# Kernel tuning notes

Measured on AMD Instinct MI355X. Metric: run time of the kernel, lower is better.

Reference implementation:

```python
import jax, jax.numpy as jnp
import numpy as np

EMBED_DIM = 2048
HEAD_DIM = 128
B, T = 4, 2048


def setup_inputs() -> dict:
    key = jax.random.key(0)
    k1, k2, k3, k4 = jax.random.split(key, 4)
    x_in = jax.random.normal(k1, (B, T, EMBED_DIM), dtype=jnp.float32)
    scale = 1.0 / np.sqrt(EMBED_DIM)
    Wq = jax.random.normal(k2, (EMBED_DIM, HEAD_DIM), dtype=jnp.float32) * scale
    Wk = jax.random.normal(k3, (EMBED_DIM, HEAD_DIM), dtype=jnp.float32) * scale
    Wv = jax.random.normal(k4, (EMBED_DIM, HEAD_DIM), dtype=jnp.float32) * scale
    return {"x_in": x_in, "Wq": Wq, "Wk": Wk, "Wv": Wv}


def reference(x_in, Wq, Wk, Wv):
    # x_in: [B, T, E]; projections (Linear, no bias)
    q = jnp.einsum('bte,ed->btd', x_in, Wq)  # [B,T,D]
    k = jnp.einsum('bte,ed->btd', x_in, Wk)
    v = jnp.einsum('bte,ed->btd', x_in, Wv)
    t = x_in.shape[1]
    d = Wq.shape[1]
    s = jnp.einsum('btd,bsd->bts', q, k) / jnp.sqrt(jnp.asarray(d, q.dtype))  # [B,Tq,Tk]
    # causal mask: positions with tril==0 (k index > q index) -> -inf
    causal = jnp.tril(jnp.ones((t, t), dtype=bool))
    s = jnp.where(causal, s, -jnp.inf)
    # NOTE: original module applies softmax over dim=1 (query axis), faithfully reproduced
    a = jax.nn.softmax(s, axis=1)
    z = jnp.einsum('bts,bsd->btd', a, v)  # [B,T,D]
    return z
```

## Files before the change

### kernel.cpp

```cpp
#include <hip/hip_runtime.h>

typedef _Float16 f16x8 __attribute__((ext_vector_type(8)));
typedef float f32x4 __attribute__((ext_vector_type(4)));

#define T_DIM 2048
#define E_DIM 2048
#define D_DIM 128
#define NB 4
#define KSP_P 4
#define KCH_P 512
#define KSP_A 8
#define KCH_A 256
#define CH2 64
#define NCH2 (T_DIM / CH2)

__device__ __forceinline__ void gll16(const void* g, void* l) {
  __builtin_amdgcn_global_load_lds(
      (const __attribute__((address_space(1))) unsigned int*)g,
      (__attribute__((address_space(3))) unsigned int*)l, 16, 0, 0);
}

__device__ __forceinline__ void merge_stat(float& m, float& l, float pm, float pl) {
  if (pm != -__builtin_inff()) {
    float nm = fmaxf(m, pm);
    l = l * __expf(m - nm) + pl * __expf(pm - nm);
    m = nm;
  }
}


__global__ void cvt_w(const float* __restrict__ Wq, const float* __restrict__ Wk,
                      const float* __restrict__ Wv, _Float16* __restrict__ WhT) {
  int idx = blockIdx.x * 256 + threadIdx.x;
  int w = blockIdx.y;
  const float* W = (w == 0) ? Wq : ((w == 1) ? Wk : Wv);
  int e = idx & (E_DIM - 1), d = idx >> 11;
  WhT[(size_t)w * (D_DIM * E_DIM) + idx] = (_Float16)W[e * D_DIM + d];
}


__global__ __launch_bounds__(256) void proj_gemm(
    const float* __restrict__ x, const _Float16* __restrict__ WhT,
    _Float16* __restrict__ Ph) {
  __shared__ _Float16 As[128 * 32];
  __shared__ _Float16 Bs[128 * 32];
  const int tid = threadIdx.x, w = tid >> 6, lane = tid & 63;
  const int wr = w >> 1, wc = w & 1, quad = lane >> 4, l16 = lane & 15;
  const int t0 = blockIdx.x * 128;
  const int wsel = blockIdx.y, ks = blockIdx.z;
  const _Float16* B = WhT + (size_t)wsel * (D_DIM * E_DIM);
  const int srow = lane >> 2, scol = (lane & 3) * 8;
  f32x4 acc[4][4] = {};
  for (int k0 = ks * KCH_P; k0 < ks * KCH_P + KCH_P; k0 += 32) {
    __syncthreads();
#pragma unroll
    for (int q = 0; q < 2; ++q) {
      int rbase = w * 32 + q * 16;
      int row = rbase + srow;
      const float* xp = x + (size_t)(t0 + row) * E_DIM + k0 + scol;
      f32x4 a0 = *(const f32x4*)xp;
      f32x4 a1 = *(const f32x4*)(xp + 4);
      f16x8 o;
#pragma unroll
      for (int e = 0; e < 4; ++e) { o[e] = (_Float16)a0[e]; o[e + 4] = (_Float16)a1[e]; }
      *(f16x8*)(As + row * 32 + scol) = o;
      gll16(B + (size_t)row * E_DIM + k0 + scol, Bs + rbase * 32);
    }
    __syncthreads();
    f16x8 af[4], bf[4];
#pragma unroll
    for (int i = 0; i < 4; ++i)
      af[i] = *(const f16x8*)(As + (wr * 64 + i * 16 + l16) * 32 + quad * 8);
#pragma unroll
    for (int j = 0; j < 4; ++j)
      bf[j] = *(const f16x8*)(Bs + (wc * 64 + j * 16 + l16) * 32 + quad * 8);
#pragma unroll
    for (int i = 0; i < 4; ++i)
#pragma unroll
      for (int j = 0; j < 4; ++j)
        acc[i][j] = __builtin_amdgcn_mfma_f32_16x16x32_f16(af[i], bf[j], acc[i][j], 0, 0, 0);
  }
  _Float16* P = Ph + ((size_t)(ks * 3 + wsel) << 20);
#pragma unroll
  for (int i = 0; i < 4; ++i)
#pragma unroll
    for (int j = 0; j < 4; ++j) {
      int n = wc * 64 + j * 16 + l16;
#pragma unroll
      for (int r = 0; r < 4; ++r) {
        int t = t0 + wr * 64 + i * 16 + quad * 4 + r;
        _Float16 h = (_Float16)acc[i][j][r];
        if (wsel < 2) P[(size_t)t * D_DIM + n] = h;
        else P[((size_t)(t >> 11) * D_DIM + n) * T_DIM + (t & (T_DIM - 1))] = h;
      }
    }
}


__global__ void proj_reduce(const _Float16* __restrict__ Ph, _Float16* __restrict__ Qh,
                            _Float16* __restrict__ Kh, _Float16* __restrict__ VT) {
  size_t u = ((size_t)blockIdx.x * 256 + threadIdx.x) * 8;
  int mat = (int)(u >> 20);
  size_t rem = u & ((1u << 20) - 1);
  float s[8] = {};
#pragma unroll
  for (int ks = 0; ks < KSP_P; ++ks) {
    f16x8 p = *(const f16x8*)(Ph + ((size_t)(ks * 3 + mat) << 20) + rem);
#pragma unroll
    for (int e = 0; e < 8; ++e) s[e] += (float)p[e];
  }
  f16x8 o;
#pragma unroll
  for (int e = 0; e < 8; ++e) o[e] = (_Float16)s[e];
  _Float16* dst = (mat == 0) ? Qh : ((mat == 1) ? Kh : VT);
  *(f16x8*)(dst + rem) = o;
}


__global__ __launch_bounds__(256) void s_gemm(const _Float16* __restrict__ Qh,
                                              const _Float16* __restrict__ Kh,
                                              _Float16* __restrict__ S,
                                              float* __restrict__ Pm,
                                              float* __restrict__ Pl) {
  int idx = blockIdx.x;
  int xt = (int)((sqrtf(8.f * idx + 1.f) - 1.f) * 0.5f);
  while ((xt + 1) * (xt + 2) / 2 <= idx) ++xt;
  while (xt * (xt + 1) / 2 > idx) --xt;
  int yt = idx - xt * (xt + 1) / 2;
  __shared__ _Float16 As[128 * 32];
  __shared__ _Float16 Bs[128 * 32];
  const int tid = threadIdx.x, w = tid >> 6, lane = tid & 63;
  const int wr = w >> 1, wc = w & 1, quad = lane >> 4, l16 = lane & 15;
  const int t0 = xt * 128, s0 = yt * 128, b = blockIdx.y;
  const _Float16* A = Qh + (size_t)b * T_DIM * D_DIM;
  const _Float16* B = Kh + (size_t)b * T_DIM * D_DIM;
  const int srow = lane >> 2, scol = (lane & 3) * 8;
  f32x4 acc[4][4] = {};
  for (int k0 = 0; k0 < D_DIM; k0 += 32) {
    __syncthreads();
#pragma unroll
    for (int q = 0; q < 2; ++q) {
      int rbase = w * 32 + q * 16;
      gll16(A + (size_t)(t0 + rbase + srow) * D_DIM + k0 + scol, As + rbase * 32);
      gll16(B + (size_t)(s0 + rbase + srow) * D_DIM + k0 + scol, Bs + rbase * 32);
    }
    __syncthreads();
    f16x8 af[4], bf[4];
#pragma unroll
    for (int i = 0; i < 4; ++i)
      af[i] = *(const f16x8*)(As + (wr * 64 + i * 16 + l16) * 32 + quad * 8);
#pragma unroll
    for (int j = 0; j < 4; ++j)
      bf[j] = *(const f16x8*)(Bs + (wc * 64 + j * 16 + l16) * 32 + quad * 8);
#pragma unroll
    for (int i = 0; i < 4; ++i)
#pragma unroll
      for (int j = 0; j < 4; ++j)
        acc[i][j] = __builtin_amdgcn_mfma_f32_16x16x32_f16(af[i], bf[j], acc[i][j], 0, 0, 0);
  }
  _Float16* Sb = S + (size_t)b * T_DIM * T_DIM;
  const float scale = 0.08838834764831845f;
  const float NEG = -__builtin_inff();
#pragma unroll
  for (int j = 0; j < 4; ++j) {
    const int s = s0 + wc * 64 + j * 16 + l16;
    float m = NEG;
#pragma unroll
    for (int i = 0; i < 4; ++i)
#pragma unroll
      for (int r = 0; r < 4; ++r) {
        int t = t0 + wr * 64 + i * 16 + quad * 4 + r;
        float v = (s > t) ? NEG : acc[i][j][r] * scale;
        Sb[(size_t)t * T_DIM + s] = (_Float16)v;
        m = fmaxf(m, v);
      }
    float l = 0.f;
    if (m != NEG) {
#pragma unroll
      for (int i = 0; i < 4; ++i)
#pragma unroll
        for (int r = 0; r < 4; ++r) {
          int t = t0 + wr * 64 + i * 16 + quad * 4 + r;
          float v = (s > t) ? NEG : acc[i][j][r] * scale;
          l += __expf(v - m);
        }
    }
#pragma unroll
    for (int d = 16; d <= 32; d <<= 1) {
      float pm = __shfl_xor(m, d, 64);
      float pl = __shfl_xor(l, d, 64);
      merge_stat(m, l, pm, pl);
    }
    if (quad == 0) {
      int c = 2 * xt + wr;
      Pm[((size_t)c * NB + b) * T_DIM + s] = m;
      Pl[((size_t)c * NB + b) * T_DIM + s] = l;
    }
  }
}


__global__ __launch_bounds__(256) void comb_stats(const float* __restrict__ Pm,
                                                  const float* __restrict__ Pl,
                                                  float* __restrict__ M,
                                                  float* __restrict__ L) {
  __shared__ float sM[8][32];
  __shared__ float sL[8][32];
  const int g = threadIdx.x >> 5, sl = threadIdx.x & 31;
  const int c = blockIdx.x * 32 + sl;
  const int b = c >> 11, s = c & (T_DIM - 1);
  float m = -__builtin_inff(), l = 0.f;
#pragma unroll
  for (int k = 0; k < NCH2 / 8; ++k) {
    int ch = g * (NCH2 / 8) + k;
    if (ch >= (s >> 6)) {
      size_t idx = ((size_t)ch * NB + b) * T_DIM + s;
      merge_stat(m, l, Pm[idx], Pl[idx]);
    }
  }
  sM[g][sl] = m;
  sL[g][sl] = l;
  __syncthreads();
  if (threadIdx.x < 32) {
    const int c2 = blockIdx.x * 32 + threadIdx.x;
    float fm = -__builtin_inff(), fl = 0.f;
#pragma unroll
    for (int gg = 0; gg < 8; ++gg) merge_stat(fm, fl, sM[gg][threadIdx.x], sL[gg][threadIdx.x]);
    M[c2] = fm;
    L[c2] = 1.f / fl;
  }
}


__global__ __launch_bounds__(256) void av_gemm(const _Float16* __restrict__ S,
                                               const _Float16* __restrict__ VT,
                                               const float* __restrict__ M,
                                               const float* __restrict__ L,
                                               float* __restrict__ Zp) {
  const int t0 = blockIdx.x * 128, b = blockIdx.y, ks = blockIdx.z;
  const int Kmax = t0 + 128;
  const int Kstart = ks * KCH_A;
  if (Kstart >= Kmax) return;
  const int Kend = (Kstart + KCH_A < Kmax) ? (Kstart + KCH_A) : Kmax;
  __shared__ _Float16 As[128 * 32];
  __shared__ _Float16 Bs[128 * 32];
  __shared__ float Ms[KCH_A];
  __shared__ float Ls[KCH_A];
  const int tid = threadIdx.x, w = tid >> 6, lane = tid & 63;
  const int wr = w >> 1, wc = w & 1, quad = lane >> 4, l16 = lane & 15;
  const _Float16* Sb = S + (size_t)b * T_DIM * T_DIM;
  const _Float16* Vb = VT + (size_t)b * D_DIM * T_DIM;
  for (int i = tid; i < Kend - Kstart; i += 256) {
    Ms[i] = M[b * T_DIM + Kstart + i];
    Ls[i] = L[b * T_DIM + Kstart + i];
  }
  const int srow = lane >> 2, scol = (lane & 3) * 8;
  f32x4 acc[4][4] = {};
  for (int k0 = Kstart; k0 < Kend; k0 += 32) {
    __syncthreads();
#pragma unroll
    for (int q = 0; q < 2; ++q) {
      int u = q * 256 + tid;
      int row = u >> 2, c8 = (u & 3) * 8;
      int sc = k0 + c8;
      f16x8 v = *(const f16x8*)(Sb + (size_t)(t0 + row) * T_DIM + sc);
      f16x8 o;
#pragma unroll
      for (int e = 0; e < 8; ++e) {
        int li = sc + e - Kstart;
        float a = __expf((float)v[e] - Ms[li]) * Ls[li];
        o[e] = (_Float16)a;
      }
      *(f16x8*)(As + row * 32 + c8) = o;
      int rbase = w * 32 + q * 16;
      gll16(Vb + (size_t)(rbase + srow) * T_DIM + k0 + scol, Bs + rbase * 32);
    }
    __syncthreads();
    f16x8 af[4], bf[4];
#pragma unroll
    for (int i = 0; i < 4; ++i)
      af[i] = *(const f16x8*)(As + (wr * 64 + i * 16 + l16) * 32 + quad * 8);
#pragma unroll
    for (int j = 0; j < 4; ++j)
      bf[j] = *(const f16x8*)(Bs + (wc * 64 + j * 16 + l16) * 32 + quad * 8);
#pragma unroll
    for (int i = 0; i < 4; ++i)
#pragma unroll
      for (int j = 0; j < 4; ++j)
        acc[i][j] = __builtin_amdgcn_mfma_f32_16x16x32_f16(af[i], bf[j], acc[i][j], 0, 0, 0);
  }
  float* Zb = Zp + ((size_t)ks * NB + b) * T_DIM * D_DIM;
#pragma unroll
  for (int i = 0; i < 4; ++i)
#pragma unroll
    for (int j = 0; j < 4; ++j) {
      int n = wc * 64 + j * 16 + l16;
#pragma unroll
      for (int r = 0; r < 4; ++r) {
        int t = t0 + wr * 64 + i * 16 + quad * 4 + r;
        Zb[(size_t)t * D_DIM + n] = acc[i][j][r];
      }
    }
}


__global__ void z_reduce(const float* __restrict__ Zp, float* __restrict__ Z) {
  size_t flat = ((size_t)blockIdx.x * 256 + threadIdx.x) * 4;
  int t = (int)((flat >> 7) & (T_DIM - 1));
  int ns = ((t >> 7) + 2) >> 1;
  f32x4 s = {};
  for (int ks = 0; ks < ns; ++ks) {
    f32x4 p = *(const f32x4*)(Zp + ((size_t)ks * NB * T_DIM * D_DIM) + flat);
    s += p;
  }
  *(f32x4*)(Z + flat) = s;
}


extern "C" void kernel_launch(void* const* d_in, const int* in_sizes, int n_in,
                              void* d_out, int out_size, void* d_ws, size_t ws_size,
                              hipStream_t stream) {
  const float* x = (const float*)d_in[0];
  const float* Wq = (const float*)d_in[1];
  const float* Wk = (const float*)d_in[2];
  const float* Wv = (const float*)d_in[3];
  char* ws = (char*)d_ws;
  float* Zp = (float*)(ws);
  _Float16* WhT = (_Float16*)(ws + 33554432);
  _Float16* Qh = (_Float16*)(ws + 35127296);
  _Float16* Kh = (_Float16*)(ws + 37224448);
  _Float16* VT = (_Float16*)(ws + 39321600);
  _Float16* S = (_Float16*)(ws + 41418752);
  _Float16* Ph = (_Float16*)(ws + 41418752);
  float* M = (float*)(ws + 74973184);
  float* L = (float*)(ws + 75005952);
  float* Pm = (float*)(ws + 75038720);
  float* Pl = (float*)(ws + 76087296);
  float* Z = (float*)d_out;

  cvt_w<<<dim3(1024, 3), 256, 0, stream>>>(Wq, Wk, Wv, WhT);
  proj_gemm<<<dim3(64, 3, KSP_P), 256, 0, stream>>>(x, WhT, Ph);
  proj_reduce<<<1536, 256, 0, stream>>>(Ph, Qh, Kh, VT);
  s_gemm<<<dim3(136, 4), 256, 0, stream>>>(Qh, Kh, S, Pm, Pl);
  comb_stats<<<256, 256, 0, stream>>>(Pm, Pl, M, L);
  av_gemm<<<dim3(16, 4, KSP_A), 256, 0, stream>>>(S, VT, M, L, Zp);
  z_reduce<<<1024, 256, 0, stream>>>(Zp, Z);
}
```

Baseline: 178.4 us.

## Enlarge projection GEMM row tile to 256 and double K split

The projection GEMM now computes 256 rows per block instead of 128, so each B tile of fp16 weights loaded into LDS is reused across twice as many rows. The K dimension is split 8 ways instead of 4 to keep the block count unchanged. The partial-sum buffers are spread over two workspace regions, one of which reuses the Zp area, and the reduce kernel reads eight partials. The cost is more accumulator registers (32 f32x4 per thread, with a launch bound of 2 blocks), a larger LDS footprint, and twice the partial-sum traffic in the reduction.

```diff
diff --git a/kernel.cpp b/kernel.cpp
--- a/kernel.cpp
+++ b/kernel.cpp
@@ -7,12 +7,13 @@
 #define E_DIM 2048
 #define D_DIM 128
 #define NB 4
-#define KSP_P 4
-#define KCH_P 512
+#define KSP_P 8
+#define KCH_P 256
 #define KSP_A 8
 #define KCH_A 256
 #define CH2 64
 #define NCH2 (T_DIM / CH2)
+#define PH_SLOT (1u << 20)
 
 __device__ __forceinline__ void gll16(const void* g, void* l) {
   __builtin_amdgcn_global_load_lds(
@@ -39,56 +40,62 @@
 }
 
 
-__global__ __launch_bounds__(256) void proj_gemm(
+__global__ __launch_bounds__(256, 2) void proj_gemm(
     const float* __restrict__ x, const _Float16* __restrict__ WhT,
-    _Float16* __restrict__ Ph) {
-  __shared__ _Float16 As[128 * 32];
+    _Float16* __restrict__ Ph0, _Float16* __restrict__ Ph1) {
+  __shared__ _Float16 As[256 * 32];
   __shared__ _Float16 Bs[128 * 32];
   const int tid = threadIdx.x, w = tid >> 6, lane = tid & 63;
   const int wr = w >> 1, wc = w & 1, quad = lane >> 4, l16 = lane & 15;
-  const int t0 = blockIdx.x * 128;
+  const int t0 = blockIdx.x * 256;
   const int wsel = blockIdx.y, ks = blockIdx.z;
   const _Float16* B = WhT + (size_t)wsel * (D_DIM * E_DIM);
   const int srow = lane >> 2, scol = (lane & 3) * 8;
-  f32x4 acc[4][4] = {};
+  const int arow = tid >> 2, acol = (tid & 3) * 8;
+  f32x4 acc[8][4] = {};
   for (int k0 = ks * KCH_P; k0 < ks * KCH_P + KCH_P; k0 += 32) {
     __syncthreads();
 #pragma unroll
-    for (int q = 0; q < 2; ++q) {
-      int rbase = w * 32 + q * 16;
-      int row = rbase + srow;
-      const float* xp = x + (size_t)(t0 + row) * E_DIM + k0 + scol;
+    for (int p = 0; p < 4; ++p) {
+      int row = p * 64 + arow;
+      const float* xp = x + (size_t)(t0 + row) * E_DIM + k0 + acol;
       f32x4 a0 = *(const f32x4*)xp;
       f32x4 a1 = *(const f32x4*)(xp + 4);
       f16x8 o;
 #pragma unroll
       for (int e = 0; e < 4; ++e) { o[e] = (_Float16)a0[e]; o[e + 4] = (_Float16)a1[e]; }
-      *(f16x8*)(As + row * 32 + scol) = o;
-      gll16(B + (size_t)row * E_DIM + k0 + scol, Bs + rbase * 32);
-    }
-    __syncthreads();
-    f16x8 af[4], bf[4];
-#pragma unroll
-    for (int i = 0; i < 4; ++i)
-      af[i] = *(const f16x8*)(As + (wr * 64 + i * 16 + l16) * 32 + quad * 8);
+      *(f16x8*)(As + row * 32 + acol) = o;
+    }
+#pragma unroll
+    for (int q = 0; q < 2; ++q) {
+      int rbase = w * 32 + q * 16;
+      gll16(B + (size_t)(rbase + srow) * E_DIM + k0 + scol, Bs + rbase * 32);
+    }
+    __syncthreads();
+    f16x8 af[8], bf[4];
+#pragma unroll
+    for (int i = 0; i < 8; ++i)
+      af[i] = *(const f16x8*)(As + (wr * 128 + i * 16 + l16) * 32 + quad * 8);
 #pragma unroll
     for (int j = 0; j < 4; ++j)
       bf[j] = *(const f16x8*)(Bs + (wc * 64 + j * 16 + l16) * 32 + quad * 8);
 #pragma unroll
-    for (int i = 0; i < 4; ++i)
+    for (int i = 0; i < 8; ++i)
 #pragma unroll
       for (int j = 0; j < 4; ++j)
         acc[i][j] = __builtin_amdgcn_mfma_f32_16x16x32_f16(af[i], bf[j], acc[i][j], 0, 0, 0);
   }
-  _Float16* P = Ph + ((size_t)(ks * 3 + wsel) << 20);
-#pragma unroll
-  for (int i = 0; i < 4; ++i)
+  const int slot = ks * 3 + wsel;
+  _Float16* P = (slot < 12) ? (Ph0 + ((size_t)slot << 20))
+                            : (Ph1 + ((size_t)(slot - 12) << 20));
+#pragma unroll
+  for (int i = 0; i < 8; ++i)
 #pragma unroll
     for (int j = 0; j < 4; ++j) {
       int n = wc * 64 + j * 16 + l16;
 #pragma unroll
       for (int r = 0; r < 4; ++r) {
-        int t = t0 + wr * 64 + i * 16 + quad * 4 + r;
+        int t = t0 + wr * 128 + i * 16 + quad * 4 + r;
         _Float16 h = (_Float16)acc[i][j][r];
         if (wsel < 2) P[(size_t)t * D_DIM + n] = h;
         else P[((size_t)(t >> 11) * D_DIM + n) * T_DIM + (t & (T_DIM - 1))] = h;
@@ -97,7 +104,9 @@
 }
 
 
-__global__ void proj_reduce(const _Float16* __restrict__ Ph, _Float16* __restrict__ Qh,
+__global__ void proj_reduce(const _Float16* __restrict__ Ph0,
+                            const _Float16* __restrict__ Ph1,
+                            _Float16* __restrict__ Qh,
                             _Float16* __restrict__ Kh, _Float16* __restrict__ VT) {
   size_t u = ((size_t)blockIdx.x * 256 + threadIdx.x) * 8;
   int mat = (int)(u >> 20);
@@ -105,7 +114,10 @@
   float s[8] = {};
 #pragma unroll
   for (int ks = 0; ks < KSP_P; ++ks) {
-    f16x8 p = *(const f16x8*)(Ph + ((size_t)(ks * 3 + mat) << 20) + rem);
+    int slot = ks * 3 + mat;
+    const _Float16* P = (slot < 12) ? (Ph0 + ((size_t)slot << 20))
+                                    : (Ph1 + ((size_t)(slot - 12) << 20));
+    f16x8 p = *(const f16x8*)(P + rem);
 #pragma unroll
     for (int e = 0; e < 8; ++e) s[e] += (float)p[e];
   }
@@ -326,12 +338,13 @@
   const float* Wv = (const float*)d_in[3];
   char* ws = (char*)d_ws;
   float* Zp = (float*)(ws);
+  _Float16* Ph0 = (_Float16*)(ws);
   _Float16* WhT = (_Float16*)(ws + 33554432);
   _Float16* Qh = (_Float16*)(ws + 35127296);
   _Float16* Kh = (_Float16*)(ws + 37224448);
   _Float16* VT = (_Float16*)(ws + 39321600);
   _Float16* S = (_Float16*)(ws + 41418752);
-  _Float16* Ph = (_Float16*)(ws + 41418752);
+  _Float16* Ph1 = (_Float16*)(ws + 41418752);
   float* M = (float*)(ws + 74973184);
   float* L = (float*)(ws + 75005952);
   float* Pm = (float*)(ws + 75038720);
@@ -339,8 +352,8 @@
   float* Z = (float*)d_out;
 
   cvt_w<<<dim3(1024, 3), 256, 0, stream>>>(Wq, Wk, Wv, WhT);
-  proj_gemm<<<dim3(64, 3, KSP_P), 256, 0, stream>>>(x, WhT, Ph);
-  proj_reduce<<<1536, 256, 0, stream>>>(Ph, Qh, Kh, VT);
+  proj_gemm<<<dim3(32, 3, KSP_P), 256, 0, stream>>>(x, WhT, Ph0, Ph1);
+  proj_reduce<<<1536, 256, 0, stream>>>(Ph0, Ph1, Qh, Kh, VT);
   s_gemm<<<dim3(136, 4), 256, 0, stream>>>(Qh, Kh, S, Pm, Pl);
   comb_stats<<<256, 256, 0, stream>>>(Pm, Pl, M, L);
   av_gemm<<<dim3(16, 4, KSP_A), 256, 0, stream>>>(S, VT, M, L, Zp);
```

New measurement: 213.1 us. 1.19x slower.

## Load A operands directly into registers and deepen B staging in projection and S GEMMs

Applied to the files above, without the earlier changes.

In the projection GEMM, the x tile is no longer staged through LDS. Each wave loads its fp32 rows from global memory straight into MFMA fragments, and the K step doubles to 64 with two B buffers, which halves the barrier count. In the S GEMM, all four K slices of the K tile are staged in LDS up front with one barrier, and the Q fragments are read directly from global memory. The V-transpose store is vectorized to 4-wide halves. This removes LDS traffic and synchronisation but relies on uncoalesced-ish direct global fragment loads, and the NCH2 macro change may affect code not shown.

```diff
diff --git a/kernel.cpp b/kernel.cpp
--- a/kernel.cpp
+++ b/kernel.cpp
@@ -1,6 +1,7 @@
 #include <hip/hip_runtime.h>
 
 typedef _Float16 f16x8 __attribute__((ext_vector_type(8)));
+typedef _Float16 f16x4 __attribute__((ext_vector_type(4)));
 typedef float f32x4 __attribute__((ext_vector_type(4)));
 
 #define T_DIM 2048
@@ -11,8 +12,7 @@
 #define KCH_P 512
 #define KSP_A 8
 #define KCH_A 256
-#define CH2 64
-#define NCH2 (T_DIM / CH2)
+#define NCH2 32
 
 __device__ __forceinline__ void gll16(const void* g, void* l) {
   __builtin_amdgcn_global_load_lds(
@@ -42,8 +42,7 @@
 __global__ __launch_bounds__(256) void proj_gemm(
     const float* __restrict__ x, const _Float16* __restrict__ WhT,
     _Float16* __restrict__ Ph) {
-  __shared__ _Float16 As[128 * 32];
-  __shared__ _Float16 Bs[128 * 32];
+  __shared__ _Float16 Bs[2][128 * 32];
   const int tid = threadIdx.x, w = tid >> 6, lane = tid & 63;
   const int wr = w >> 1, wc = w & 1, quad = lane >> 4, l16 = lane & 15;
   const int t0 = blockIdx.x * 128;
@@ -51,49 +50,68 @@
   const _Float16* B = WhT + (size_t)wsel * (D_DIM * E_DIM);
   const int srow = lane >> 2, scol = (lane & 3) * 8;
   f32x4 acc[4][4] = {};
-  for (int k0 = ks * KCH_P; k0 < ks * KCH_P + KCH_P; k0 += 32) {
+  for (int k0 = ks * KCH_P; k0 < ks * KCH_P + KCH_P; k0 += 64) {
     __syncthreads();
 #pragma unroll
-    for (int q = 0; q < 2; ++q) {
-      int rbase = w * 32 + q * 16;
-      int row = rbase + srow;
-      const float* xp = x + (size_t)(t0 + row) * E_DIM + k0 + scol;
-      f32x4 a0 = *(const f32x4*)xp;
-      f32x4 a1 = *(const f32x4*)(xp + 4);
-      f16x8 o;
-#pragma unroll
-      for (int e = 0; e < 4; ++e) { o[e] = (_Float16)a0[e]; o[e + 4] = (_Float16)a1[e]; }
-      *(f16x8*)(As + row * 32 + scol) = o;
-      gll16(B + (size_t)row * E_DIM + k0 + scol, Bs + rbase * 32);
-    }
+    for (int h = 0; h < 2; ++h)
+#pragma unroll
+      for (int q = 0; q < 2; ++q) {
+        int rbase = w * 32 + q * 16;
+        gll16(B + (size_t)(rbase + srow) * E_DIM + k0 + h * 32 + scol,
+              Bs[h] + rbase * 32);
+      }
     __syncthreads();
-    f16x8 af[4], bf[4];
-#pragma unroll
-    for (int i = 0; i < 4; ++i)
-      af[i] = *(const f16x8*)(As + (wr * 64 + i * 16 + l16) * 32 + quad * 8);
-#pragma unroll
-    for (int j = 0; j < 4; ++j)
-      bf[j] = *(const f16x8*)(Bs + (wc * 64 + j * 16 + l16) * 32 + quad * 8);
-#pragma unroll
-    for (int i = 0; i < 4; ++i)
+#pragma unroll
+    for (int h = 0; h < 2; ++h) {
+      f16x8 af[4], bf[4];
+#pragma unroll
+      for (int i = 0; i < 4; ++i) {
+        const float* xp = x + (size_t)(t0 + wr * 64 + i * 16 + l16) * E_DIM +
+                          k0 + h * 32 + quad * 8;
+        f32x4 a0 = *(const f32x4*)xp;
+        f32x4 a1 = *(const f32x4*)(xp + 4);
+#pragma unroll
+        for (int e = 0; e < 4; ++e) {
+          af[i][e] = (_Float16)a0[e];
+          af[i][e + 4] = (_Float16)a1[e];
+        }
+      }
 #pragma unroll
       for (int j = 0; j < 4; ++j)
-        acc[i][j] = __builtin_amdgcn_mfma_f32_16x16x32_f16(af[i], bf[j], acc[i][j], 0, 0, 0);
+        bf[j] = *(const f16x8*)(Bs[h] + (wc * 64 + j * 16 + l16) * 32 + quad * 8);
+#pragma unroll
+      for (int i = 0; i < 4; ++i)
+#pragma unroll
+        for (int j = 0; j < 4; ++j)
+          acc[i][j] = __builtin_amdgcn_mfma_f32_16x16x32_f16(af[i], bf[j], acc[i][j], 0, 0, 0);
+    }
   }
   _Float16* P = Ph + ((size_t)(ks * 3 + wsel) << 20);
-#pragma unroll
-  for (int i = 0; i < 4; ++i)
-#pragma unroll
-    for (int j = 0; j < 4; ++j) {
-      int n = wc * 64 + j * 16 + l16;
-#pragma unroll
-      for (int r = 0; r < 4; ++r) {
-        int t = t0 + wr * 64 + i * 16 + quad * 4 + r;
-        _Float16 h = (_Float16)acc[i][j][r];
-        if (wsel < 2) P[(size_t)t * D_DIM + n] = h;
-        else P[((size_t)(t >> 11) * D_DIM + n) * T_DIM + (t & (T_DIM - 1))] = h;
-      }
-    }
+  if (wsel < 2) {
+#pragma unroll
+    for (int i = 0; i < 4; ++i)
+#pragma unroll
+      for (int j = 0; j < 4; ++j) {
+        int n = wc * 64 + j * 16 + l16;
+#pragma unroll
+        for (int r = 0; r < 4; ++r) {
+          int t = t0 + wr * 64 + i * 16 + quad * 4 + r;
+          P[(size_t)t * D_DIM + n] = (_Float16)acc[i][j][r];
+        }
+      }
+  } else {
+#pragma unroll
+    for (int i = 0; i < 4; ++i)
+#pragma unroll
+      for (int j = 0; j < 4; ++j) {
+        int n = wc * 64 + j * 16 + l16;
+        int t = t0 + wr * 64 + i * 16 + quad * 4;
+        f16x4 o;
+#pragma unroll
+        for (int r = 0; r < 4; ++r) o[r] = (_Float16)acc[i][j][r];
+        *(f16x4*)(P + ((size_t)(t >> 11) * D_DIM + n) * T_DIM + (t & (T_DIM - 1))) = o;
+      }
+  }
 }
 
 
@@ -127,31 +145,33 @@
   while ((xt + 1) * (xt + 2) / 2 <= idx) ++xt;
   while (xt * (xt + 1) / 2 > idx) --xt;
   int yt = idx - xt * (xt + 1) / 2;
-  __shared__ _Float16 As[128 * 32];
-  __shared__ _Float16 Bs[128 * 32];
+  __shared__ _Float16 Bs[4][128 * 32];
   const int tid = threadIdx.x, w = tid >> 6, lane = tid & 63;
   const int wr = w >> 1, wc = w & 1, quad = lane >> 4, l16 = lane & 15;
   const int t0 = xt * 128, s0 = yt * 128, b = blockIdx.y;
   const _Float16* A = Qh + (size_t)b * T_DIM * D_DIM;
   const _Float16* B = Kh + (size_t)b * T_DIM * D_DIM;
   const int srow = lane >> 2, scol = (lane & 3) * 8;
-  f32x4 acc[4][4] = {};
-  for (int k0 = 0; k0 < D_DIM; k0 += 32) {
-    __syncthreads();
+#pragma unroll
+  for (int kq = 0; kq < 4; ++kq)
 #pragma unroll
     for (int q = 0; q < 2; ++q) {
       int rbase = w * 32 + q * 16;
-      gll16(A + (size_t)(t0 + rbase + srow) * D_DIM + k0 + scol, As + rbase * 32);
-      gll16(B + (size_t)(s0 + rbase + srow) * D_DIM + k0 + scol, Bs + rbase * 32);
-    }
-    __syncthreads();
+      gll16(B + (size_t)(s0 + rbase + srow) * D_DIM + kq * 32 + scol,
+            Bs[kq] + rbase * 32);
+    }
+  __syncthreads();
+  f32x4 acc[4][4] = {};
+#pragma unroll
+  for (int kq = 0; kq < 4; ++kq) {
     f16x8 af[4], bf[4];
 #pragma unroll
     for (int i = 0; i < 4; ++i)
-      af[i] = *(const f16x8*)(As + (wr * 64 + i * 16 + l16) * 32 + quad * 8);
+      af[i] = *(const f16x8*)(A + (size_t)(t0 + wr * 64 + i * 16 + l16) * D_DIM +
+                              kq * 32 + quad * 8);
 #pragma unroll
     for (int j = 0; j < 4; ++j)
-      bf[j] = *(const f16x8*)(Bs + (wc * 64 + j * 16 + l16) * 32 + quad * 8);
+      bf[j] = *(const f16x8*)(Bs[kq] + (wc * 64 + j * 16 + l16) * 32 + quad * 8);
 #pragma unroll
     for (int i = 0; i < 4; ++i)
 #pragma unroll
```

Result: slower. 202.0 us (+13.2%).
